# Kernel tuning notes

Hardware: AMD Instinct MI355X
Metric: run time of the kernel (lower is better)

The kernel has to match this reference:

```python
import jax, jax.numpy as jnp
import numpy as np

N = 50000   # nodes
HID = 32    # hidden_channels
H = 8       # heads == num_edge_features (positional-arg aliasing in source)
E = 800000  # message-passing edges
L = 100000  # supervision (label) edges
NEG_SLOPE = 0.2


def gat_layer(x, src, dst, edge_attr, W, a_src, a_dst, We, a_e, b):
    # x: [N, Fin]; W: [Fin, H*C] -> out [N, H*C] (concat heads), PyG GATConv math
    C = W.shape[1] // H
    h = (x @ W).reshape(-1, H, C)                 # [N, H, C]
    al_src = (h * a_src).sum(-1)                  # [N, H]
    al_dst = (h * a_dst).sum(-1)                  # [N, H]
    he = (edge_attr @ We).reshape(-1, H, C)       # [E, H, C]
    al_e = (he * a_e).sum(-1)                     # [E, H]
    alpha = al_src[src] + al_dst[dst] + al_e      # [E, H]
    alpha = jax.nn.leaky_relu(alpha, NEG_SLOPE)
    # segment softmax over destination-node neighborhoods
    amax = jax.ops.segment_max(alpha, dst, num_segments=N)
    amax = jnp.where(jnp.isfinite(amax), amax, 0.0)
    ex = jnp.exp(alpha - amax[dst])
    denom = jax.ops.segment_sum(ex, dst, num_segments=N)
    w = ex / (denom[dst] + 1e-16)                 # [E, H]
    out = jax.ops.segment_sum(h[src] * w[:, :, None], dst, num_segments=N)
    return out.reshape(-1, H * C) + b             # [N, H*C]


def setup_inputs():
    key = jax.random.key(0)
    ks = jax.random.split(key, 24)
    s = 0.1
    d = {}
    d["node_ids"] = jax.random.randint(ks[0], (N,), 0, N)
    d["edge_index"] = jax.random.randint(ks[1], (2, E), 0, N)
    d["edge_label_index"] = jax.random.randint(ks[2], (2, L), 0, N)
    d["topic"] = jax.random.randint(ks[3], (1,), 0, 10)
    d["edge_attr"] = jax.random.normal(ks[4], (E, H))
    d["edge_label_attr"] = jax.random.normal(ks[5], (L, H))
    d["emb"] = jax.random.normal(ks[6], (N, HID)) * s
    d["W1"] = jax.random.normal(ks[7], (HID, H * HID)) * s
    d["a_src1"] = jax.random.normal(ks[8], (H, HID)) * s
    d["a_dst1"] = jax.random.normal(ks[9], (H, HID)) * s
    d["We1"] = jax.random.normal(ks[10], (H, H * HID)) * s
    d["a_e1"] = jax.random.normal(ks[11], (H, HID)) * s
    d["b1"] = jnp.zeros((H * HID,))
    d["lin1_W"] = jax.random.normal(ks[12], (H * HID, HID)) * s
    d["lin1_b"] = jnp.zeros((HID,))
    d["W2"] = jax.random.normal(ks[13], (HID, H * HID)) * s
    d["a_src2"] = jax.random.normal(ks[14], (H, HID)) * s
    d["a_dst2"] = jax.random.normal(ks[15], (H, HID)) * s
    d["We2"] = jax.random.normal(ks[16], (H, H * HID)) * s
    d["a_e2"] = jax.random.normal(ks[17], (H, HID)) * s
    d["b2"] = jnp.zeros((H * HID,))
    d["lin5_W"] = jax.random.normal(ks[18], (H * HID, H)) * s
    d["lin5_b"] = jnp.zeros((H,))
    d["clf_W"] = jax.random.normal(ks[19], (2 * H, H)) * s
    d["clf_b"] = jnp.zeros((H,))
    return d


def reference(node_ids, edge_index, edge_label_index, topic, edge_attr, edge_label_attr, emb, W1, a_src1, a_dst1, We1, a_e1, b1, lin1_W, lin1_b, W2, a_src2, a_dst2, We2, a_e2, b2, lin5_W, lin5_b, clf_W, clf_b):
    src, dst = edge_index[0], edge_index[1]
    x = emb[node_ids]                                                   # [N, HID]
    x = jax.nn.relu(gat_layer(x, src, dst, edge_attr, W1, a_src1, a_dst1, We1, a_e1, b1))
    x = x @ lin1_W + lin1_b                                             # dropout(p=0.1) is identity in eval
    x = jax.nn.relu(gat_layer(x, src, dst, edge_attr, W2, a_src2, a_dst2, We2, a_e2, b2))
    x = x @ lin5_W + lin5_b                                             # [N, H]
    fu = x[edge_label_index[0]]                                         # [L, H]
    fm = x[edge_label_index[1]]                                         # [L, H]
    fu = jnp.concatenate([fu, edge_label_attr], axis=-1) @ clf_W + clf_b
    return jax.nn.sigmoid((fu * fm).sum(-1))                            # [L]
```

## Files before the change

kernel.cpp:

```cpp
#include <hip/hip_runtime.h>
#include <hip/hip_bf16.h>

#define HC    256
#define FIN   32
#define NH    8
#define GROUP 8
#define CAPW  32

typedef __hip_bfloat16 bf16;

__device__ __forceinline__ float blo(unsigned int u) { return __uint_as_float(u << 16); }
__device__ __forceinline__ float bhi(unsigned int u) { return __uint_as_float(u & 0xffff0000u); }
__device__ __forceinline__ unsigned int pk2(float a, float b) {
  bf16 ha = __float2bfloat16(a), hb = __float2bfloat16(b);
  unsigned short ua, ub;
  __builtin_memcpy(&ua, &ha, 2); __builtin_memcpy(&ub, &hb, 2);
  return (unsigned int)ua | ((unsigned int)ub << 16);
}

__global__ void count_kernel(const int* __restrict__ dst, int* __restrict__ cnt,
                             int* __restrict__ ord, int E_) {
  int e = blockIdx.x * blockDim.x + threadIdx.x;
  if (e < E_) ord[e] = atomicAdd(&cnt[dst[e]], 1);
}

__global__ __launch_bounds__(256) void
scan_partial(const int* __restrict__ cnt, int* __restrict__ tmp,
             int* __restrict__ bsum, int N_) {
  __shared__ int part[256];
  int t = threadIdx.x, i = blockIdx.x * 256 + t;
  int v = (i < N_) ? cnt[i] : 0;
  part[t] = v;
  __syncthreads();
#pragma unroll
  for (int off = 1; off < 256; off <<= 1) {
    int u = (t >= off) ? part[t - off] : 0;
    __syncthreads();
    part[t] += u;
    __syncthreads();
  }
  if (i < N_) tmp[i] = part[t];
  if (t == 255) bsum[blockIdx.x] = part[255];
}

__global__ __launch_bounds__(1024) void
scan_bsum_fold(int* __restrict__ bsum, int NB,
               const float* __restrict__ We1, const float* __restrict__ ae1,
               const float* __restrict__ We2, const float* __restrict__ ae2,
               const float* __restrict__ W1, const float* __restrict__ as1,
               const float* __restrict__ ad1,
               const float* __restrict__ W2, const float* __restrict__ as2,
               const float* __restrict__ ad2,
               float* __restrict__ M) {
  __shared__ int part[1024];
  int t = threadIdx.x;
  int v = (t < NB) ? bsum[t] : 0;
  part[t] = v;
  __syncthreads();
  for (int off = 1; off < 1024; off <<= 1) {
    int u = (t >= off) ? part[t - off] : 0;
    __syncthreads();
    part[t] += u;
    __syncthreads();
  }
  if (t < NB) bsum[t] = part[t] - v;

  for (int idx = t; idx < 1152; idx += 1024) {
    const float* A; const float* V; int i;
    if (idx < 64)       { i = idx;       A = We1; V = ae1; }
    else if (idx < 128) { i = idx - 64;  A = We2; V = ae2; }
    else if (idx < 384) { i = idx - 128; A = W1;  V = as1; }
    else if (idx < 640) { i = idx - 384; A = W1;  V = ad1; }
    else if (idx < 896) { i = idx - 640; A = W2;  V = as2; }
    else                { i = idx - 896; A = W2;  V = ad2; }
    int k = i >> 3, h = i & 7;
    float s = 0.f;
    for (int c = 0; c < FIN; ++c)
      s = fmaf(A[k * HC + h * FIN + c], V[h * FIN + c], s);
    M[idx] = s;
  }
}

__global__ __launch_bounds__(256) void
scan_final(const int* __restrict__ cnt, const int* __restrict__ tmp,
           const int* __restrict__ bsum, int* __restrict__ rowptr,
           int N_, int E_) {
  int t = threadIdx.x, i = blockIdx.x * 256 + t;
  if (i < N_) rowptr[i] = bsum[blockIdx.x] + tmp[i] - cnt[i];
  if (i == 0) rowptr[N_] = E_;
}

__global__ __launch_bounds__(256) void
scatter_prep_kernel(const int* __restrict__ src, const int* __restrict__ dst,
                    const int* __restrict__ rowptr, const int* __restrict__ ord,
                    const float* __restrict__ edge_attr, const float* __restrict__ M,
                    int* __restrict__ srcs, unsigned int* __restrict__ alepk,
                    const float* __restrict__ emb, const int* __restrict__ node_ids,
                    bf16* __restrict__ xq, float* __restrict__ alsrc,
                    float* __restrict__ aldst,
                    int E_, int N_, int eb) {
  __shared__ float Msh[128];
  __shared__ float xs[8][33];
  int t = threadIdx.x;
  if (blockIdx.x < eb) {
    if (t < 128) Msh[t] = M[t];
    __syncthreads();
    int e = blockIdx.x * 256 + t;
    if (e < E_) {
      int pos = rowptr[dst[e]] + ord[e];
      srcs[pos] = src[e];
      const float4* ep = (const float4*)(edge_attr + (size_t)e * NH);
      float4 a0 = ep[0], a1 = ep[1];
      float ea[8] = {a0.x, a0.y, a0.z, a0.w, a1.x, a1.y, a1.z, a1.w};
      float o1[8], o2[8];
#pragma unroll
      for (int h = 0; h < 8; ++h) { o1[h] = 0.f; o2[h] = 0.f; }
#pragma unroll
      for (int k = 0; k < 8; ++k) {
        float x = ea[k];
#pragma unroll
        for (int h = 0; h < 8; ++h) {
          o1[h] = fmaf(x, Msh[k * 8 + h], o1[h]);
          o2[h] = fmaf(x, Msh[64 + k * 8 + h], o2[h]);
        }
      }
      uint4 r0 = make_uint4(pk2(o1[0], o1[1]), pk2(o1[2], o1[3]),
                            pk2(o1[4], o1[5]), pk2(o1[6], o1[7]));
      uint4 r1 = make_uint4(pk2(o2[0], o2[1]), pk2(o2[2], o2[3]),
                            pk2(o2[4], o2[5]), pk2(o2[6], o2[7]));
      uint4* op = (uint4*)(alepk + (size_t)pos * 8);
      op[0] = r0; op[1] = r1;
    }
  } else {
    const float* P = M + 128;
    int n0 = (blockIdx.x - eb) * 8;
    int nl = t >> 5, c = t & 31;
    int n = n0 + nl;
    if (n < N_) {
      float v = emb[(size_t)node_ids[n] * FIN + c];
      xq[(size_t)n * FIN + c] = __float2bfloat16(v);
      xs[nl][c] = v;
    }
    __syncthreads();
    if (t < 64) {
      int nl2 = t >> 3, h = t & 7;
      int n2 = n0 + nl2;
      if (n2 < N_) {
        float sa = 0.f, sd = 0.f;
#pragma unroll
        for (int k = 0; k < FIN; ++k) {
          float x = xs[nl2][k];
          sa = fmaf(x, P[k * 8 + h], sa);
          sd = fmaf(x, P[256 + k * 8 + h], sd);
        }
        alsrc[(size_t)n2 * NH + h] = sa;
        aldst[(size_t)n2 * NH + h] = sd;
      }
    }
  }
}

template <int K, int LOG2K, bool LOGITS>
__global__ __launch_bounds__(256, 8) void
agg_kernel(const int* __restrict__ rowptr, const int* __restrict__ srcs,
           const bf16* __restrict__ ale,
           const float* __restrict__ alsrc, const float* __restrict__ aldst,
           const bf16* __restrict__ xq,
           const float* __restrict__ W, const float* __restrict__ b,
           const float* __restrict__ Wlin, const float* __restrict__ blin,
           float* __restrict__ xoutf, bf16* __restrict__ xqn,
           const float* __restrict__ Pn,
           float* __restrict__ alsrcn, float* __restrict__ aldstn, int N_) {
  __shared__ __align__(16) char smem[17408];
  unsigned int* xsu = (unsigned int*)smem;
  float* wsf   = (float*)(smem + 8192);
  float* ald_s = (float*)(smem + 12288);
  float* zs   = (float*)smem;
  float* gs   = (float*)(smem + 8192);
  float* red  = (float*)smem;
  float* xrow = (float*)(smem + 16384);

  int t = threadIdx.x;
  int n0 = blockIdx.x * GROUP;
  int w = t >> 6, l = t & 63, h = l >> 3, q = l & 7;

  unsigned int* xw  = xsu + w * 512;
  float*        wsw = wsf + w * 256;

  int nA = n0 + w * 2;
  int e0  = rowptr[(nA     <= N_) ? nA     : N_];
  int e1  = rowptr[(nA + 1 <= N_) ? nA + 1 : N_];
  int e2g = rowptr[(nA + 2 <= N_) ? nA + 2 : N_];

  if (t < GROUP * NH) {
    int nn = n0 + (t >> 3);
    ald_s[t] = (nn < N_) ? aldst[(size_t)nn * NH + (t & 7)] : 0.f;
  }
  __syncthreads();

  float4 acc0 = make_float4(0.f, 0.f, 0.f, 0.f);
  float4 acc1 = make_float4(0.f, 0.f, 0.f, 0.f);
  float dn0 = 0.f, dn1 = 0.f;

  for (int cbeg = e0; cbeg < e2g; cbeg += CAPW) {
    int clen = e2g - cbeg; if (clen > CAPW) clen = CAPW;

    int ntask = clen * 8;
    for (int idx = l; idx < ntask; idx += 64) {
      int e = idx >> 3, c4 = idx & 7;
      int s = srcs[cbeg + e];
      uint2 v = *(const uint2*)(xq + (size_t)s * FIN + c4 * 4);
      *(uint2*)&xw[e * 16 + c4 * 2] = v;
    }
    {
      int e2 = l >> 1, half = l & 1;
      if (e2 < clen) {
        int j = cbeg + e2;
        int ii = (j >= e1) ? 1 : 0;
        int sn = srcs[j];
        uint2 ue  = *(const uint2*)(ale + (size_t)j * 16 + half * 4);
        float4 as4 = *(const float4*)(alsrc + (size_t)sn * NH + half * 4);
        float4 ad4 = *(const float4*)&ald_s[(w * 2 + ii) * 8 + half * 4];
        float a0f = blo(ue.x) + as4.x + ad4.x; a0f = (a0f >= 0.f) ? a0f : 0.2f * a0f;
        float a1f = bhi(ue.x) + as4.y + ad4.y; a1f = (a1f >= 0.f) ? a1f : 0.2f * a1f;
        float a2f = blo(ue.y) + as4.z + ad4.z; a2f = (a2f >= 0.f) ? a2f : 0.2f * a2f;
        float a3f = bhi(ue.y) + as4.w + ad4.w; a3f = (a3f >= 0.f) ? a3f : 0.2f * a3f;
        *(float4*)&wsw[e2 * 8 + half * 4] =
            make_float4(__expf(a0f), __expf(a1f), __expf(a2f), __expf(a3f));
      }
    }
    asm volatile("s_waitcnt lgkmcnt(0)" ::: "memory");

    int hA = e1 - cbeg; if (hA < 0) hA = 0; if (hA > clen) hA = clen;
#pragma unroll 4
    for (int le = 0; le < hA; ++le) {
      float wv = wsw[le * 8 + h];
      uint2 u = *(const uint2*)&xw[le * 16 + q * 2];
      acc0.x = fmaf(blo(u.x), wv, acc0.x);
      acc0.y = fmaf(bhi(u.x), wv, acc0.y);
      acc0.z = fmaf(blo(u.y), wv, acc0.z);
      acc0.w = fmaf(bhi(u.y), wv, acc0.w);
      dn0 += wv;
    }
#pragma unroll 4
    for (int le = hA; le < clen; ++le) {
      float wv = wsw[le * 8 + h];
      uint2 u = *(const uint2*)&xw[le * 16 + q * 2];
      acc1.x = fmaf(blo(u.x), wv, acc1.x);
      acc1.y = fmaf(bhi(u.x), wv, acc1.y);
      acc1.z = fmaf(blo(u.y), wv, acc1.z);
      acc1.w = fmaf(bhi(u.y), wv, acc1.w);
      dn1 += wv;
    }
    asm volatile("s_waitcnt lgkmcnt(0)" ::: "memory");
  }

  float rd0 = 1.0f / (dn0 + 1e-16f);
  float rd1 = 1.0f / (dn1 + 1e-16f);
  *(float4*)&zs[(w * 2 + 0) * 256 + l * 4] =
      make_float4(acc0.x * rd0, acc0.y * rd0, acc0.z * rd0, acc0.w * rd0);
  *(float4*)&zs[(w * 2 + 1) * 256 + l * 4] =
      make_float4(acc1.x * rd1, acc1.y * rd1, acc1.z * rd1, acc1.w * rd1);
  __syncthreads();

  int hE = t >> 5;
  float g[GROUP];
#pragma unroll
  for (int i = 0; i < GROUP; ++i) g[i] = b[t];
#pragma unroll
  for (int k4 = 0; k4 < 8; ++k4) {
    float za[GROUP][4];
#pragma unroll
    for (int i = 0; i < GROUP; ++i)
      *(float4*)za[i] = *(const float4*)&zs[i * 256 + hE * 32 + k4 * 4];
#pragma unroll
    for (int kk = 0; kk < 4; ++kk) {
      float wv = W[(k4 * 4 + kk) * HC + t];
#pragma unroll
      for (int i = 0; i < GROUP; ++i) g[i] = fmaf(za[i][kk], wv, g[i]);
    }
  }
  __syncthreads();
#pragma unroll
  for (int i = 0; i < GROUP; ++i) gs[i * 256 + t] = (g[i] > 0.f) ? g[i] : 0.f;
  __syncthreads();

  {
    int kk = t & (K - 1), r = t >> LOG2K;
    float part[GROUP];
#pragma unroll
    for (int i = 0; i < GROUP; ++i) part[i] = 0.f;
#pragma unroll
    for (int j4 = 0; j4 < K / 4; ++j4) {
      float ga[GROUP][4];
#pragma unroll
      for (int i = 0; i < GROUP; ++i)
        *(float4*)ga[i] = *(const float4*)&gs[i * 256 + r * K + j4 * 4];
#pragma unroll
      for (int jj = 0; jj < 4; ++jj) {
        float wl = Wlin[(r * K + j4 * 4 + jj) * K + kk];
#pragma unroll
        for (int i = 0; i < GROUP; ++i) part[i] = fmaf(ga[i][jj], wl, part[i]);
      }
    }
#pragma unroll
    for (int i = 0; i < GROUP; ++i) red[i * 256 + t] = part[i];
  }
  __syncthreads();

  if (LOGITS) {
    if (t < GROUP * 32) {
      int i = t >> 5, kk = t & 31;
      float s = blin[kk];
#pragma unroll
      for (int r2 = 0; r2 < HC / K; ++r2) s += red[i * 256 + r2 * K + kk];
      int nn = n0 + i;
      if (nn < N_) xqn[(size_t)nn * FIN + kk] = __float2bfloat16(s);
      xrow[t] = s;
    }
    __syncthreads();
    if (t < GROUP * NH) {
      int i = t >> 3, hh = t & 7;
      int nn = n0 + i;
      if (nn < N_) {
        float sa = 0.f, sd = 0.f;
#pragma unroll
        for (int k2 = 0; k2 < FIN; ++k2) {
          float x = xrow[i * 32 + k2];
          sa = fmaf(x, Pn[k2 * 8 + hh], sa);
          sd = fmaf(x, Pn[256 + k2 * 8 + hh], sd);
        }
        alsrcn[(size_t)nn * NH + hh] = sa;
        aldstn[(size_t)nn * NH + hh] = sd;
      }
    }
  } else {
    if (t < GROUP * K) {
      int i = t >> LOG2K, kk = t & (K - 1);
      float s = blin[kk];
#pragma unroll
      for (int r2 = 0; r2 < HC / K; ++r2) s += red[i * 256 + r2 * K + kk];
      int nn = n0 + i;
      if (nn < N_) xoutf[(size_t)nn * K + kk] = s;
    }
  }
}

__global__ void clf_kernel(const int* __restrict__ eli, const float* __restrict__ ela,
                           const float* __restrict__ x2, const float* __restrict__ clfW,
                           const float* __restrict__ clfb, float* __restrict__ out, int L_) {
  int i = blockIdx.x * blockDim.x + threadIdx.x;
  if (i >= L_) return;
  int u = eli[i], m = eli[L_ + i];
  const float4* xup = (const float4*)(x2 + (size_t)u * NH);
  const float4* xmp = (const float4*)(x2 + (size_t)m * NH);
  const float4* eap = (const float4*)(ela + (size_t)i * NH);
  float4 xu0 = xup[0], xu1 = xup[1];
  float4 xm0 = xmp[0], xm1 = xmp[1];
  float4 el0 = eap[0], el1 = eap[1];
  float xu[NH] = {xu0.x, xu0.y, xu0.z, xu0.w, xu1.x, xu1.y, xu1.z, xu1.w};
  float xm[NH] = {xm0.x, xm0.y, xm0.z, xm0.w, xm1.x, xm1.y, xm1.z, xm1.w};
  float el[NH] = {el0.x, el0.y, el0.z, el0.w, el1.x, el1.y, el1.z, el1.w};
  float fu[NH];
#pragma unroll
  for (int kk = 0; kk < NH; ++kk) fu[kk] = clfb[kk];
#pragma unroll
  for (int j = 0; j < NH; ++j) {
#pragma unroll
    for (int kk = 0; kk < NH; ++kk) fu[kk] = fmaf(xu[j], clfW[j * NH + kk], fu[kk]);
  }
#pragma unroll
  for (int j = 0; j < NH; ++j) {
#pragma unroll
    for (int kk = 0; kk < NH; ++kk) fu[kk] = fmaf(el[j], clfW[(NH + j) * NH + kk], fu[kk]);
  }
  float dot = 0.f;
#pragma unroll
  for (int kk = 0; kk < NH; ++kk) dot += fu[kk] * xm[kk];
  out[i] = 1.f / (1.f + expf(-dot));
}

extern "C" void kernel_launch(void* const* d_in, const int* in_sizes, int n_in,
                              void* d_out, int out_size, void* d_ws, size_t ws_size,
                              hipStream_t stream) {
  const int* node_ids   = (const int*)d_in[0];
  const int* edge_index = (const int*)d_in[1];
  const int* eli        = (const int*)d_in[2];
  const float* edge_attr = (const float*)d_in[4];
  const float* ela       = (const float*)d_in[5];
  const float* emb       = (const float*)d_in[6];
  const float* W1     = (const float*)d_in[7];
  const float* a_src1 = (const float*)d_in[8];
  const float* a_dst1 = (const float*)d_in[9];
  const float* We1    = (const float*)d_in[10];
  const float* a_e1   = (const float*)d_in[11];
  const float* b1     = (const float*)d_in[12];
  const float* lin1W  = (const float*)d_in[13];
  const float* lin1b  = (const float*)d_in[14];
  const float* W2     = (const float*)d_in[15];
  const float* a_src2 = (const float*)d_in[16];
  const float* a_dst2 = (const float*)d_in[17];
  const float* We2    = (const float*)d_in[18];
  const float* a_e2   = (const float*)d_in[19];
  const float* b2     = (const float*)d_in[20];
  const float* lin5W  = (const float*)d_in[21];
  const float* lin5b  = (const float*)d_in[22];
  const float* clfW   = (const float*)d_in[23];
  const float* clfb   = (const float*)d_in[24];

  const int N_ = in_sizes[0];
  const int E_ = in_sizes[1] / 2;
  const int L_ = in_sizes[2] / 2;
  const int* src  = edge_index;
  const int* dstp = edge_index + E_;

  char* p = (char*)d_ws;
  auto carve = [&](size_t bytes) -> char* {
    char* r = p;
    p += (bytes + 255) & ~(size_t)255;
    return r;
  };
  bf16*  xq1     = (bf16*)carve((size_t)N_ * FIN * 2);
  bf16*  xq2     = (bf16*)carve((size_t)N_ * FIN * 2);
  unsigned int* alepk = (unsigned int*)carve((size_t)E_ * 32);
  float* alsrc1  = (float*)carve((size_t)N_ * NH * 4);
  float* aldst1  = (float*)carve((size_t)N_ * NH * 4);
  float* alsrc2  = (float*)carve((size_t)N_ * NH * 4);
  float* aldst2  = (float*)carve((size_t)N_ * NH * 4);
  float* x2b     = (float*)carve((size_t)N_ * NH * 4);
  float* Mbuf    = (float*)carve(1152 * 4);
  int*   cnt     = (int*)carve((size_t)N_ * 4);
  int*   rowptr  = (int*)carve((size_t)(N_ + 1) * 4);
  int*   stmp    = (int*)carve((size_t)N_ * 4);
  int*   bsum    = (int*)carve(1024 * 4);
  int*   srcs    = (int*)carve((size_t)E_ * 4);
  int*   ordb    = (int*)carve((size_t)E_ * 4);

  hipMemsetAsync(cnt, 0, (size_t)N_ * 4, stream);
  int eb = (E_ + 255) / 256;
  int nb = (N_ + 255) / 256;
  int pb = (N_ + 7) / 8;
  count_kernel<<<eb, 256, 0, stream>>>(dstp, cnt, ordb, E_);
  scan_partial<<<nb, 256, 0, stream>>>(cnt, stmp, bsum, N_);
  scan_bsum_fold<<<1, 1024, 0, stream>>>(bsum, nb, We1, a_e1, We2, a_e2,
                                         W1, a_src1, a_dst1, W2, a_src2, a_dst2,
                                         Mbuf);
  scan_final<<<nb, 256, 0, stream>>>(cnt, stmp, bsum, rowptr, N_, E_);
  scatter_prep_kernel<<<eb + pb, 256, 0, stream>>>(
      src, dstp, rowptr, ordb, edge_attr, Mbuf, srcs, alepk,
      emb, node_ids, xq1, alsrc1, aldst1, E_, N_, eb);

  int gb = (N_ + GROUP - 1) / GROUP;
  agg_kernel<32, 5, true><<<gb, 256, 0, stream>>>(
      rowptr, srcs, (const bf16*)alepk, alsrc1, aldst1, xq1,
      W1, b1, lin1W, lin1b, nullptr, xq2, Mbuf + 640, alsrc2, aldst2, N_);

  agg_kernel<8, 3, false><<<gb, 256, 0, stream>>>(
      rowptr, srcs, ((const bf16*)alepk) + 8, alsrc2, aldst2, xq2,
      W2, b2, lin5W, lin5b, x2b, nullptr, nullptr, nullptr, nullptr, N_);

  clf_kernel<<<(L_ + 255) / 256, 256, 0, stream>>>(eli, ela, x2b, clfW, clfb,
                                                   (float*)d_out, L_);
}
```

Before: 330.2 us.

## Split edge scatter into index pass plus coalesced-write alepk build; use direct global-to-LDS loads

The scatter kernel now writes only a (src, edge id) pair per sorted position. A new kernel walks the sorted positions, gathers edge_attr by edge id, and writes srcs and the packed bf16 edge logits contiguously, so the 32-byte-per-edge random writes become coalesced writes plus random 32-byte reads. Separately, the aggregation kernel stages neighbour feature rows into LDS with global_load_lds 16-byte transfers instead of going through registers, and waits on vmcnt before using them. This adds an extra kernel launch and an 8-byte-per-edge intermediate buffer. The LDS path also relies on the per-lane LDS address layout of the builtin matching the old xw indexing.

```diff
diff --git a/kernel.cpp b/kernel.cpp
--- a/kernel.cpp
+++ b/kernel.cpp
@@ -93,43 +93,19 @@
 __global__ __launch_bounds__(256) void
 scatter_prep_kernel(const int* __restrict__ src, const int* __restrict__ dst,
                     const int* __restrict__ rowptr, const int* __restrict__ ord,
-                    const float* __restrict__ edge_attr, const float* __restrict__ M,
-                    int* __restrict__ srcs, unsigned int* __restrict__ alepk,
+                    int2* __restrict__ se,
+                    const float* __restrict__ M,
                     const float* __restrict__ emb, const int* __restrict__ node_ids,
                     bf16* __restrict__ xq, float* __restrict__ alsrc,
                     float* __restrict__ aldst,
                     int E_, int N_, int eb) {
-  __shared__ float Msh[128];
   __shared__ float xs[8][33];
   int t = threadIdx.x;
   if (blockIdx.x < eb) {
-    if (t < 128) Msh[t] = M[t];
-    __syncthreads();
     int e = blockIdx.x * 256 + t;
     if (e < E_) {
       int pos = rowptr[dst[e]] + ord[e];
-      srcs[pos] = src[e];
-      const float4* ep = (const float4*)(edge_attr + (size_t)e * NH);
-      float4 a0 = ep[0], a1 = ep[1];
-      float ea[8] = {a0.x, a0.y, a0.z, a0.w, a1.x, a1.y, a1.z, a1.w};
-      float o1[8], o2[8];
-#pragma unroll
-      for (int h = 0; h < 8; ++h) { o1[h] = 0.f; o2[h] = 0.f; }
-#pragma unroll
-      for (int k = 0; k < 8; ++k) {
-        float x = ea[k];
-#pragma unroll
-        for (int h = 0; h < 8; ++h) {
-          o1[h] = fmaf(x, Msh[k * 8 + h], o1[h]);
-          o2[h] = fmaf(x, Msh[64 + k * 8 + h], o2[h]);
-        }
-      }
-      uint4 r0 = make_uint4(pk2(o1[0], o1[1]), pk2(o1[2], o1[3]),
-                            pk2(o1[4], o1[5]), pk2(o1[6], o1[7]));
-      uint4 r1 = make_uint4(pk2(o2[0], o2[1]), pk2(o2[2], o2[3]),
-                            pk2(o2[4], o2[5]), pk2(o2[6], o2[7]));
-      uint4* op = (uint4*)(alepk + (size_t)pos * 8);
-      op[0] = r0; op[1] = r1;
+      se[pos] = make_int2(src[e], e);
     }
   } else {
     const float* P = M + 128;
@@ -158,6 +134,42 @@
       }
     }
   }
+}
+
+__global__ __launch_bounds__(256) void
+alepk_build_kernel(const int2* __restrict__ se, const float* __restrict__ edge_attr,
+                   const float* __restrict__ M,
+                   int* __restrict__ srcs, unsigned int* __restrict__ alepk, int E_) {
+  __shared__ float Msh[128];
+  int t = threadIdx.x;
+  if (t < 128) Msh[t] = M[t];
+  __syncthreads();
+  int pos = blockIdx.x * 256 + t;
+  if (pos >= E_) return;
+  int2 s2 = se[pos];
+  srcs[pos] = s2.x;
+  int e = s2.y;
+  const float4* ep = (const float4*)(edge_attr + (size_t)e * NH);
+  float4 a0 = ep[0], a1 = ep[1];
+  float ea[8] = {a0.x, a0.y, a0.z, a0.w, a1.x, a1.y, a1.z, a1.w};
+  float o1[8], o2[8];
+#pragma unroll
+  for (int h = 0; h < 8; ++h) { o1[h] = 0.f; o2[h] = 0.f; }
+#pragma unroll
+  for (int k = 0; k < 8; ++k) {
+    float x = ea[k];
+#pragma unroll
+    for (int h = 0; h < 8; ++h) {
+      o1[h] = fmaf(x, Msh[k * 8 + h], o1[h]);
+      o2[h] = fmaf(x, Msh[64 + k * 8 + h], o2[h]);
+    }
+  }
+  uint4 r0 = make_uint4(pk2(o1[0], o1[1]), pk2(o1[2], o1[3]),
+                        pk2(o1[4], o1[5]), pk2(o1[6], o1[7]));
+  uint4 r1 = make_uint4(pk2(o2[0], o2[1]), pk2(o2[2], o2[3]),
+                        pk2(o2[4], o2[5]), pk2(o2[6], o2[7]));
+  uint4* op = (uint4*)(alepk + (size_t)pos * 8);
+  op[0] = r0; op[1] = r1;
 }
 
 template <int K, int LOG2K, bool LOGITS>
@@ -186,6 +198,7 @@
 
   unsigned int* xw  = xsu + w * 512;
   float*        wsw = wsf + w * 256;
+  char* xwb = smem + w * 2048;
 
   int nA = n0 + w * 2;
   int e0  = rowptr[(nA     <= N_) ? nA     : N_];
@@ -205,12 +218,26 @@
   for (int cbeg = e0; cbeg < e2g; cbeg += CAPW) {
     int clen = e2g - cbeg; if (clen > CAPW) clen = CAPW;
 
-    int ntask = clen * 8;
-    for (int idx = l; idx < ntask; idx += 64) {
-      int e = idx >> 3, c4 = idx & 7;
-      int s = srcs[cbeg + e];
-      uint2 v = *(const uint2*)(xq + (size_t)s * FIN + c4 * 4);
-      *(uint2*)&xw[e * 16 + c4 * 2] = v;
+    {
+      int el0 = (l >> 2);
+      int coff = (l & 3);
+      int ec0 = el0 < clen - 1 ? el0 : clen - 1;
+      {
+        int s = srcs[cbeg + ec0];
+        const bf16* gp = xq + (size_t)s * FIN + coff * 8;
+        __builtin_amdgcn_global_load_lds(
+            (const __attribute__((address_space(1))) void*)gp,
+            (__attribute__((address_space(3))) void*)xwb, 16, 0, 0);
+      }
+      if (clen > 16) {
+        int el1 = 16 + el0;
+        int ec1 = el1 < clen - 1 ? el1 : clen - 1;
+        int s = srcs[cbeg + ec1];
+        const bf16* gp = xq + (size_t)s * FIN + coff * 8;
+        __builtin_amdgcn_global_load_lds(
+            (const __attribute__((address_space(1))) void*)gp,
+            (__attribute__((address_space(3))) void*)(xwb + 1024), 16, 0, 0);
+      }
     }
     {
       int e2 = l >> 1, half = l & 1;
@@ -229,7 +256,7 @@
             make_float4(__expf(a0f), __expf(a1f), __expf(a2f), __expf(a3f));
       }
     }
-    asm volatile("s_waitcnt lgkmcnt(0)" ::: "memory");
+    asm volatile("s_waitcnt vmcnt(0) lgkmcnt(0)" ::: "memory");
 
     int hA = e1 - cbeg; if (hA < 0) hA = 0; if (hA > clen) hA = clen;
 #pragma unroll 4
@@ -435,6 +462,7 @@
   int*   bsum    = (int*)carve(1024 * 4);
   int*   srcs    = (int*)carve((size_t)E_ * 4);
   int*   ordb    = (int*)carve((size_t)E_ * 4);
+  int2*  se      = (int2*)carve((size_t)E_ * 8);
 
   hipMemsetAsync(cnt, 0, (size_t)N_ * 4, stream);
   int eb = (E_ + 255) / 256;
@@ -447,8 +475,9 @@
                                          Mbuf);
   scan_final<<<nb, 256, 0, stream>>>(cnt, stmp, bsum, rowptr, N_, E_);
   scatter_prep_kernel<<<eb + pb, 256, 0, stream>>>(
-      src, dstp, rowptr, ordb, edge_attr, Mbuf, srcs, alepk,
+      src, dstp, rowptr, ordb, se, Mbuf,
       emb, node_ids, xq1, alsrc1, aldst1, E_, N_, eb);
+  alepk_build_kernel<<<eb, 256, 0, stream>>>(se, edge_attr, Mbuf, srcs, alepk, E_);
 
   int gb = (N_ + GROUP - 1) / GROUP;
   agg_kernel<32, 5, true><<<gb, 256, 0, stream>>>(
```

Result: faster. 319.8 us (-3.2%).
